# Performance work log

Measured on AMD Instinct MI355X. Metric: run time of the kernel, lower is better.

Reference implementation:

```python
import jax, jax.numpy as jnp
import numpy as np

H = 2  # num_heads hardcoded in the torch module


def setup_inputs() -> dict:
    key = jax.random.key(0)
    ks = jax.random.split(key, 10)
    B, S, D = 8, 2048, 512
    s = 0.02
    return {
        "rgb": jax.random.normal(ks[0], (B, S, D), jnp.float32),
        "event": jax.random.normal(ks[1], (B, S, D), jnp.float32),
        "w_rgb": jax.random.normal(ks[2], (D, D), jnp.float32) * s,
        "b_rgb": jnp.zeros((D,), jnp.float32),
        "w_event": jax.random.normal(ks[3], (D, D), jnp.float32) * s,
        "b_event": jnp.zeros((D,), jnp.float32),
        "w_in": jax.random.normal(ks[4], (3 * D, D), jnp.float32) * s,   # packed QKV in_proj, torch layout
        "b_in": jnp.zeros((3 * D,), jnp.float32),
        "w_out": jax.random.normal(ks[5], (D, D), jnp.float32) * s,
        "b_out": jnp.zeros((D,), jnp.float32),
    }


def _mha(q_in, kv_in, w_in, b_in, w_out, b_out):
    """torch nn.MultiheadAttention with key==value==kv_in, batch-first math."""
    B, S, D = q_in.shape
    hd = D // H
    q = q_in @ w_in[:D].T + b_in[:D]
    k = kv_in @ w_in[D:2 * D].T + b_in[D:2 * D]
    v = kv_in @ w_in[2 * D:].T + b_in[2 * D:]
    q = q.reshape(B, S, H, hd) * (1.0 / np.sqrt(hd))
    k = k.reshape(B, S, H, hd)
    v = v.reshape(B, S, H, hd)
    scores = jnp.einsum('bqhd,bkhd->bhqk', q, k)          # [B,H,S,S]
    attn = jax.nn.softmax(scores, axis=-1)
    out = jnp.einsum('bhqk,bkhd->bqhd', attn, v).reshape(B, S, D)
    return out @ w_out.T + b_out


def reference(rgb, event, w_rgb, b_rgb, w_event, b_event, w_in, b_in, w_out, b_out):
    rgb_p = rgb @ w_rgb.T + b_rgb
    event_p = event @ w_event.T + b_event
    # same attention weights used for both cross directions
    event_attn = _mha(rgb_p, event_p, w_in, b_in, w_out, b_out)
    rgb_attn = _mha(event_p, rgb_p, w_in, b_in, w_out, b_out)
    gate = jax.nn.sigmoid(jnp.sum(rgb_p * event_p, axis=-1, keepdims=True))
    fused = gate * event_attn + (1.0 - gate) * rgb_attn
    return fused + (rgb_p + event_p) * 0.5
```

## Files before the change

kernel.cpp:

```cpp
#include <hip/hip_runtime.h>
#include <hip/hip_bf16.h>
#include <stdint.h>


typedef __bf16 bf16_t;
typedef __bf16 bf16x8 __attribute__((ext_vector_type(8)));
typedef float f32x4 __attribute__((ext_vector_type(4)));
typedef float f32x16 __attribute__((ext_vector_type(16)));
typedef unsigned int u32;
typedef unsigned char u8;

typedef void gvoid_t __attribute__((address_space(1)));
typedef void svoid_t __attribute__((address_space(3)));

__device__ inline void gload16(const void* g, void* l) {
    __builtin_amdgcn_global_load_lds((gvoid_t*)g, (svoid_t*)l, 16, 0, 0);
}

__device__ inline float exp2v(float x) {
    float r;
    asm("v_exp_f32 %0, %1" : "=v"(r) : "v"(x));
    return r;
}

template <bool HI>
__device__ inline u32 pk_fp8(float a, float b, u32 old) {
    return (u32)__builtin_amdgcn_cvt_pk_fp8_f32(a, b, (int)old, HI);
}
__device__ inline u8 to_fp8(float a) { return (u8)(pk_fp8<false>(a, a, 0) & 0xff); }
__device__ inline long pk64(u32 lo, u32 hi) {
    return (long)(((unsigned long long)hi << 32) | (unsigned long long)lo);
}
__device__ inline f32x16 mfma_fp8(long a, long b, f32x16 c) {
    return __builtin_amdgcn_mfma_f32_32x32x16_fp8_fp8(a, b, c, 0, 0, 0);
}

__global__ __launch_bounds__(256) void f2b_w(const float* __restrict__ s2, bf16_t* __restrict__ d2,
                                             const float* __restrict__ s3, bf16_t* __restrict__ d3,
                                             const float* __restrict__ s4, bf16_t* __restrict__ d4,
                                             const float* __restrict__ s5, bf16_t* __restrict__ d5) {
    int i = blockIdx.x * 256 + threadIdx.x;
    const float* s; bf16_t* d; int off;
    if (i < 32768)       { s = s2; d = d2; off = i; }
    else if (i < 65536)  { s = s3; d = d3; off = i - 32768; }
    else if (i < 163840) { s = s4; d = d4; off = i - 65536; }
    else                 { s = s5; d = d5; off = i - 163840; }
    const float4* p = reinterpret_cast<const float4*>(s) + (size_t)off * 2;
    float4 a = p[0], b = p[1];
    bf16x8 o;
    o[0] = (bf16_t)a.x; o[1] = (bf16_t)a.y; o[2] = (bf16_t)a.z; o[3] = (bf16_t)a.w;
    o[4] = (bf16_t)b.x; o[5] = (bf16_t)b.y; o[6] = (bf16_t)b.z; o[7] = (bf16_t)b.w;
    reinterpret_cast<bf16x8*>(d)[off] = o;
}

template <int MODE>
__global__ __launch_bounds__(256) void gemm_bt(const float* __restrict__ Af,
                                               const float* __restrict__ Af2,
                                               const bf16_t* __restrict__ A,
                                               const bf16_t* __restrict__ A2,
                                               const bf16_t* __restrict__ Bw,
                                               const bf16_t* __restrict__ Bw2,
                                               const float* __restrict__ bias,
                                               const float* __restrict__ bias2,
                                               void* __restrict__ Cout,
                                               void* __restrict__ Cout2,
                                               const bf16_t* __restrict__ r1,
                                               const bf16_t* __restrict__ r2,
                                               const float* __restrict__ gate,
                                               u8* __restrict__ qdst,
                                               u8* __restrict__ kdst,
                                               u8* __restrict__ vdst,
                                               u8* __restrict__ qdst2,
                                               u8* __restrict__ kdst2,
                                               u8* __restrict__ vdst2,
                                               int N, int K) {
    __shared__ __align__(16) bf16_t As[128][64];
    __shared__ __align__(16) bf16_t Bs[128][64];
    const int tid = threadIdx.x, lane = tid & 63, w = tid >> 6;
    const int l16 = lane & 15, l4 = lane >> 4;
    const int wm = w >> 1, wn = w & 1;
    int xt, yt;
    if (MODE == 1) {
        int bid = blockIdx.x;
        int xcd = bid & 7, idx = bid >> 3;
        yt = xcd + 8 * (idx / 12);
        xt = idx % 12;
    } else {
        xt = blockIdx.x; yt = blockIdx.y;
    }
    const bool sec = (MODE != 2) && (yt >= 128);
    const size_t a0 = (size_t)(yt & 127) * 128;
    const size_t b0 = (size_t)xt * 128;
    const bf16_t* Ap = sec ? A2 : A;
    const bf16_t* Bp = sec ? Bw2 : Bw;
    const float* Afp = sec ? Af2 : Af;
    const float* bp = sec ? bias2 : bias;
    f32x4 acc[4][4] = {};
    const int srow = w * 32 + (lane >> 3);
    const int scol = (lane & 7) * 8;
    float g4[4];
    if (MODE == 2) {
#pragma unroll
        for (int i = 0; i < 4; ++i) g4[i] = gate[a0 + srow + i * 8];
    }
    for (int kt = 0; kt < K; kt += 64) {
        __syncthreads();
        if (MODE == 0) {
#pragma unroll
            for (int i = 0; i < 4; ++i) {
                const float4* p = reinterpret_cast<const float4*>(
                    Afp + (a0 + srow + i * 8) * (size_t)K + kt + scol);
                float4 x = p[0], y = p[1];
                bf16x8 o;
                o[0] = (bf16_t)x.x; o[1] = (bf16_t)x.y; o[2] = (bf16_t)x.z; o[3] = (bf16_t)x.w;
                o[4] = (bf16_t)y.x; o[5] = (bf16_t)y.y; o[6] = (bf16_t)y.z; o[7] = (bf16_t)y.w;
                *reinterpret_cast<bf16x8*>(&As[srow + i * 8][scol]) = o;
            }
        } else if (MODE == 2) {
#pragma unroll
            for (int i = 0; i < 4; ++i) {
                size_t ro = (a0 + srow + i * 8) * (size_t)K + kt + scol;
                bf16x8 x = *reinterpret_cast<const bf16x8*>(A + ro);
                bf16x8 y = *reinterpret_cast<const bf16x8*>(A2 + ro);
                bf16x8 o;
#pragma unroll
                for (int j = 0; j < 8; ++j)
                    o[j] = (bf16_t)(g4[i] * (float)x[j] + (1.f - g4[i]) * (float)y[j]);
                *reinterpret_cast<bf16x8*>(&As[srow + i * 8][scol]) = o;
            }
        } else {
#pragma unroll
            for (int i = 0; i < 4; ++i)
                gload16(Ap + (a0 + srow + i * 8) * (size_t)K + kt + scol, &As[w * 32 + i * 8][0]);
        }
#pragma unroll
        for (int i = 0; i < 4; ++i)
            gload16(Bp + (b0 + srow + i * 8) * (size_t)K + kt + scol, &Bs[w * 32 + i * 8][0]);
        __syncthreads();
#pragma unroll
        for (int kk = 0; kk < 2; ++kk) {
            bf16x8 af[4], bfr[4];
#pragma unroll
            for (int mi = 0; mi < 4; ++mi)
                af[mi] = *reinterpret_cast<const bf16x8*>(&As[wm * 64 + mi * 16 + l16][kk * 32 + l4 * 8]);
#pragma unroll
            for (int ni = 0; ni < 4; ++ni)
                bfr[ni] = *reinterpret_cast<const bf16x8*>(&Bs[wn * 64 + ni * 16 + l16][kk * 32 + l4 * 8]);
#pragma unroll
            for (int mi = 0; mi < 4; ++mi)
#pragma unroll
                for (int ni = 0; ni < 4; ++ni)
                    acc[mi][ni] = __builtin_amdgcn_mfma_f32_16x16x32_bf16(af[mi], bfr[ni], acc[mi][ni], 0, 0, 0);
        }
    }
    u8* qd = sec ? qdst2 : qdst;
    u8* kd = sec ? kdst2 : kdst;
    u8* vd = sec ? vdst2 : vdst;
#pragma unroll
    for (int mi = 0; mi < 4; ++mi) {
#pragma unroll
        for (int ni = 0; ni < 4; ++ni) {
            int col = (int)b0 + wn * 64 + ni * 16 + l16;
            float bs = bp[col];
            int row0 = (int)a0 + wm * 64 + mi * 16 + l4 * 4;
            float vv[4];
#pragma unroll
            for (int r = 0; r < 4; ++r) vv[r] = acc[mi][ni][r] + bs;
            if (MODE == 0) {
                bf16_t* Cp = (bf16_t*)(sec ? Cout2 : Cout);
#pragma unroll
                for (int r = 0; r < 4; ++r)
                    Cp[(size_t)(row0 + r) * N + col] = (bf16_t)vv[r];
            } else if (MODE == 2) {
#pragma unroll
                for (int r = 0; r < 4; ++r) {
                    size_t idx = (size_t)(row0 + r) * N + col;
                    ((float*)Cout)[idx] = vv[r] + 0.5f * ((float)r1[idx] + (float)r2[idx]);
                }
            } else {
                if (col < 512) {
#pragma unroll
                    for (int r = 0; r < 4; ++r)
                        qd[(size_t)(row0 + r) * 512 + col] = to_fp8(vv[r]);
                } else if (col < 1024) {
                    int cc = col - 512, hh = cc >> 8, d = cc & 255;
                    int dpart = ((d >> 3) & 1) * 128 + (d >> 4) * 8 + (d & 7);
#pragma unroll
                    for (int r = 0; r < 4; ++r) {
                        int row = row0 + r;
                        int bh = (row >> 11) * 2 + hh, seq = row & 2047;
                        int rr = seq & 31;
                        u32 boff = (u32)(rr * 256 + dpart) ^ (u32)((rr & 7) << 4);
                        kd[((size_t)(bh * 64 + (seq >> 5))) * 8192 + boff] = to_fp8(vv[r]);
                    }
                } else {
                    int cc = col - 1024, hh = cc >> 8, d = cc & 255;
                    int bh = (row0 >> 11) * 2 + hh, seq = row0 & 2047;
                    int k = seq & 31;
                    int s = (k >> 4) & 1, hik = (k >> 3) & 1, j0 = k & 7;
                    u32 wrd = pk_fp8<false>(vv[0], vv[1], 0);
                    wrd = pk_fp8<true>(vv[2], vv[3], wrd);
                    u32 boff = (u32)(d * 32 + hik * 16 + s * 8 + j0) ^ (u32)((d & 7) << 4);
                    *reinterpret_cast<u32*>(vd + ((size_t)(bh * 64 + (seq >> 5))) * 8192 + boff) = wrd;
                }
            }
        }
    }
}

__global__ __launch_bounds__(256) void gate_kernel(const bf16_t* __restrict__ rp,
                                                   const bf16_t* __restrict__ ep,
                                                   float* __restrict__ gate) {
    int row = blockIdx.x * 4 + (threadIdx.x >> 6);
    int lane = threadIdx.x & 63;
    bf16x8 a = reinterpret_cast<const bf16x8*>(rp + (size_t)row * 512)[lane];
    bf16x8 b = reinterpret_cast<const bf16x8*>(ep + (size_t)row * 512)[lane];
    float s = 0.f;
#pragma unroll
    for (int j = 0; j < 8; ++j) s += (float)a[j] * (float)b[j];
#pragma unroll
    for (int off = 32; off; off >>= 1) s += __shfl_xor(s, off, 64);
    if (lane == 0) gate[row] = 1.f / (1.f + __expf(-s));
}

__global__ __launch_bounds__(256, 2) void attn_kernel(const u8* __restrict__ qbr,
                                                      const u8* __restrict__ qbe,
                                                      const u8* __restrict__ kbr,
                                                      const u8* __restrict__ kbe,
                                                      const u8* __restrict__ vbr,
                                                      const u8* __restrict__ vbe,
                                                      bf16_t* __restrict__ out0,
                                                      bf16_t* __restrict__ out1) {
    __shared__ __align__(16) u8 smem[32768];
    const int bid = blockIdx.x;
    const int qb = bid >> 5;
    const int combo = bid & 31;
    const int dir = combo >> 4;
    const int bh = combo & 15;
    const int b = bh >> 1, h = bh & 1;
    const u8* Qb = dir ? qbe : qbr;
    const u8* Kc = dir ? kbr : kbe;
    const u8* Vc = dir ? vbr : vbe;
    bf16_t* osrc = dir ? out1 : out0;
    const int tid = threadIdx.x;
    const int w = tid >> 6, l = tid & 63;
    const int l31 = l & 31, hi = l >> 5;
    const int q0w = qb * 128 + w * 32;

    const u8* qp = Qb + ((size_t)(b * 2048 + q0w + l31)) * 512 + h * 256 + hi * 8;
    uint2 qf[16];
#pragma unroll
    for (int dch = 0; dch < 16; ++dch)
        qf[dch] = *reinterpret_cast<const uint2*>(qp + dch * 16);

    f32x16 O[8] = {};
    float mrun = -1e30f, lrun = 0.f;

    const u8* kq = Kc + (size_t)bh * 524288 + w * 2048 + l * 16;
    const u8* vq = Vc + (size_t)bh * 524288 + w * 2048 + l * 16;

#define STAGE(T, P)                                                          \
    do {                                                                     \
        const u8* ks_ = kq + (size_t)(T) * 8192;                             \
        const u8* vs_ = vq + (size_t)(T) * 8192;                             \
        gload16(ks_, &smem[(P) * 16384 + w * 2048]);                         \
        gload16(ks_ + 1024, &smem[(P) * 16384 + w * 2048 + 1024]);           \
        gload16(vs_, &smem[(P) * 16384 + 8192 + w * 2048]);                  \
        gload16(vs_ + 1024, &smem[(P) * 16384 + 8192 + w * 2048 + 1024]);    \
    } while (0)

    STAGE(0, 0);

    const u32 kx = (u32)((l31 & 7) << 4);
    for (int kt2 = 0; kt2 < 64; ++kt2) {
        asm volatile("s_waitcnt vmcnt(0)" ::: "memory");
        __builtin_amdgcn_s_barrier();
        if (kt2 < 63) STAGE(kt2 + 1, (kt2 + 1) & 1);

        const int cb = kt2 & 1;
        const u8* kbp = &smem[cb * 16384] + l31 * 256 + hi * 128;
        const u8* vg = &smem[cb * 16384 + 8192] + (((u32)(l31 * 32 + hi * 16)) ^ kx);

        f32x16 st = {};
        __builtin_amdgcn_s_setprio(1);
#pragma unroll
        for (int m = 0; m < 8; ++m) {
            uint4 kk = *reinterpret_cast<const uint4*>(kbp + (((u32)(m << 4)) ^ kx));
            st = mfma_fp8(pk64(kk.x, kk.y), pk64(qf[2 * m].x, qf[2 * m].y), st);
            st = mfma_fp8(pk64(kk.z, kk.w), pk64(qf[2 * m + 1].x, qf[2 * m + 1].y), st);
        }
        __builtin_amdgcn_s_setprio(0);

#pragma unroll
        for (int r = 0; r < 16; ++r) st[r] *= 0.090168440f;

        float mx = st[0];
#pragma unroll
        for (int r = 1; r < 16; ++r) mx = fmaxf(mx, st[r]);
        mx = fmaxf(mx, __shfl_xor(mx, 32, 64));
        if (__any(mx - mrun > 8.f)) {
            float mnew = fmaxf(mrun, mx);
            float sc = exp2v(mrun - mnew);
            mrun = mnew;
            lrun *= sc;
#pragma unroll
            for (int r = 0; r < 16; ++r) {
                int qr = (r & 3) + 8 * (r >> 2) + 4 * hi;
                float scr = __shfl(sc, qr, 64);
#pragma unroll
                for (int g = 0; g < 8; ++g) O[g][r] *= scr;
            }
        }
        float p_[16];
        float lsum = 0.f;
#pragma unroll
        for (int r = 0; r < 16; ++r) { p_[r] = exp2v(st[r] - mrun); lsum += p_[r]; }
        lsum += __shfl_xor(lsum, 32, 64);
        lrun += lsum;

        u32 X0 = pk_fp8<false>(p_[0], p_[1], 0);   X0 = pk_fp8<true>(p_[2], p_[3], X0);
        u32 X1 = pk_fp8<false>(p_[4], p_[5], 0);   X1 = pk_fp8<true>(p_[6], p_[7], X1);
        u32 X2 = pk_fp8<false>(p_[8], p_[9], 0);   X2 = pk_fp8<true>(p_[10], p_[11], X2);
        u32 X3 = pk_fp8<false>(p_[12], p_[13], 0); X3 = pk_fp8<true>(p_[14], p_[15], X3);
        u32 E0 = (u32)__shfl_xor((int)(hi ? X0 : X1), 32, 64);
        u32 E1 = (u32)__shfl_xor((int)(hi ? X2 : X3), 32, 64);
        long A0 = pk64(hi ? E0 : X0, hi ? X1 : E0);
        long A1 = pk64(hi ? E1 : X2, hi ? X3 : E1);

        __builtin_amdgcn_s_setprio(1);
#pragma unroll
        for (int g = 0; g < 8; ++g) {
            uint4 v4 = *reinterpret_cast<const uint4*>(vg + g * 1024);
            O[g] = mfma_fp8(A0, pk64(v4.x, v4.y), O[g]);
            O[g] = mfma_fp8(A1, pk64(v4.z, v4.w), O[g]);
        }
        __builtin_amdgcn_s_setprio(0);
    }
#undef STAGE

#pragma unroll
    for (int r = 0; r < 16; ++r) {
        int qr = (r & 3) + 8 * (r >> 2) + 4 * hi;
        float linv = 1.0f / __shfl(lrun, qr, 64);
        size_t rowoff = ((size_t)(b * 2048 + q0w + qr)) * 512 + h * 256 + l31;
#pragma unroll
        for (int g = 0; g < 8; ++g)
            osrc[rowoff + g * 32] = (bf16_t)(O[g][r] * linv);
    }
}

extern "C" void kernel_launch(void* const* d_in, const int* in_sizes, int n_in,
                              void* d_out, int out_size, void* d_ws, size_t ws_size,
                              hipStream_t stream) {
    const float* rgb = (const float*)d_in[0];
    const float* event = (const float*)d_in[1];
    const float* w_rgb = (const float*)d_in[2];
    const float* b_rgb = (const float*)d_in[3];
    const float* w_event = (const float*)d_in[4];
    const float* b_event = (const float*)d_in[5];
    const float* w_in = (const float*)d_in[6];
    const float* b_in = (const float*)d_in[7];
    const float* w_out = (const float*)d_in[8];
    const float* b_out = (const float*)d_in[9];
    float* out = (float*)d_out;

    const size_t MB16 = (size_t)16 * 1024 * 1024;
    char* ws = (char*)d_ws;
    bf16_t* wrgb_bf = (bf16_t*)(ws + 0);
    bf16_t* wevt_bf = (bf16_t*)(ws + 524288);
    bf16_t* wout_bf = (bf16_t*)(ws + 1048576);
    bf16_t* win_bf = (bf16_t*)(ws + 1572864);
    float* gate = (float*)(ws + 3145728);
    bf16_t* bufA = (bf16_t*)(ws + 4194304);
    bf16_t* bufB = (bf16_t*)(ws + 4194304 + MB16);
    bf16_t* rgbp = (bf16_t*)(ws + 4194304 + 2 * MB16);
    bf16_t* evtp = (bf16_t*)(ws + 4194304 + 3 * MB16);
    u8* qbr = (u8*)(ws + 4194304 + 4 * MB16);
    u8* qbe = (u8*)(ws + 4194304 + 5 * MB16);
    u8* kbr = (u8*)(ws + 4194304 + 6 * MB16);
    u8* kbe = (u8*)(ws + 4194304 + 7 * MB16);
    u8* vbr = (u8*)(ws + 4194304 + 8 * MB16);
    u8* vbe = (u8*)(ws + 4194304 + 9 * MB16);

    dim3 blk(256);
    f2b_w<<<768, blk, 0, stream>>>(w_rgb, wrgb_bf, w_event, wevt_bf,
                                   w_in, win_bf, w_out, wout_bf);
    gemm_bt<0><<<dim3(4, 256), blk, 0, stream>>>(rgb, event, nullptr, nullptr,
                                                 wrgb_bf, wevt_bf, b_rgb, b_event,
                                                 rgbp, evtp, nullptr, nullptr, nullptr,
                                                 nullptr, nullptr, nullptr, nullptr, nullptr,
                                                 nullptr, 512, 512);
    gate_kernel<<<4096, blk, 0, stream>>>(rgbp, evtp, gate);
    gemm_bt<1><<<3072, blk, 0, stream>>>(nullptr, nullptr, rgbp, evtp, win_bf, win_bf,
                                         b_in, b_in, nullptr, nullptr, nullptr, nullptr,
                                         nullptr, qbr, kbr, vbr, qbe, kbe, vbe, 1536, 512);
    attn_kernel<<<512, blk, 0, stream>>>(qbr, qbe, kbr, kbe, vbr, vbe, bufA, bufB);
    gemm_bt<2><<<dim3(4, 128), blk, 0, stream>>>(nullptr, nullptr, bufA, bufB, wout_bf, nullptr,
                                                 b_out, nullptr, out, nullptr, rgbp, evtp, gate,
                                                 nullptr, nullptr, nullptr, nullptr, nullptr,
                                                 nullptr, 512, 512);
}
```

Before: 300.9 us.

## Split K and V tile prefetch into separate stages with partial waitcnt

The attention loop now issues the K and V prefetches for the next tile separately instead of as one combined stage. Each phase waits only for the loads it needs (`vmcnt(2)`), so the V load of the current tile can still be in flight while QK^T and softmax run. This hides more global-to-LDS latency behind compute. In exchange it adds a second barrier per iteration and peels off the last iteration.

After: 306.2 us. About the same (+1.8%).

```diff
diff --git a/kernel.cpp b/kernel.cpp
--- a/kernel.cpp
+++ b/kernel.cpp
@@ -259,84 +259,112 @@
     const u8* kq = Kc + (size_t)bh * 524288 + w * 2048 + l * 16;
     const u8* vq = Vc + (size_t)bh * 524288 + w * 2048 + l * 16;
 
-#define STAGE(T, P)                                                          \
+#define SK_(T, P)                                                            \
     do {                                                                     \
         const u8* ks_ = kq + (size_t)(T) * 8192;                             \
-        const u8* vs_ = vq + (size_t)(T) * 8192;                             \
         gload16(ks_, &smem[(P) * 16384 + w * 2048]);                         \
         gload16(ks_ + 1024, &smem[(P) * 16384 + w * 2048 + 1024]);           \
+    } while (0)
+#define SV_(T, P)                                                            \
+    do {                                                                     \
+        const u8* vs_ = vq + (size_t)(T) * 8192;                             \
         gload16(vs_, &smem[(P) * 16384 + 8192 + w * 2048]);                  \
         gload16(vs_ + 1024, &smem[(P) * 16384 + 8192 + w * 2048 + 1024]);    \
     } while (0)
 
-    STAGE(0, 0);
+#define QK_PHASE(CB)                                                          \
+    do {                                                                      \
+        const u8* kbp = &smem[(CB) * 16384] + l31 * 256 + hi * 128;           \
+        __builtin_amdgcn_s_setprio(1);                                        \
+        _Pragma("unroll") for (int m = 0; m < 8; ++m) {                       \
+            uint4 kk = *reinterpret_cast<const uint4*>(kbp + (((u32)(m << 4)) ^ kx)); \
+            st = mfma_fp8(pk64(kk.x, kk.y), pk64(qf[2 * m].x, qf[2 * m].y), st); \
+            st = mfma_fp8(pk64(kk.z, kk.w), pk64(qf[2 * m + 1].x, qf[2 * m + 1].y), st); \
+        }                                                                     \
+        __builtin_amdgcn_s_setprio(0);                                        \
+    } while (0)
+
+#define SOFTMAX_PHASE()                                                       \
+    do {                                                                      \
+        _Pragma("unroll") for (int r = 0; r < 16; ++r) st[r] *= 0.090168440f; \
+        float mx = st[0];                                                     \
+        _Pragma("unroll") for (int r = 1; r < 16; ++r) mx = fmaxf(mx, st[r]); \
+        mx = fmaxf(mx, __shfl_xor(mx, 32, 64));                               \
+        if (__any(mx - mrun > 8.f)) {                                         \
+            float mnew = fmaxf(mrun, mx);                                     \
+            float sc = exp2v(mrun - mnew);                                    \
+            mrun = mnew;                                                      \
+            lrun *= sc;                                                       \
+            _Pragma("unroll") for (int r = 0; r < 16; ++r) {                  \
+                int qr = (r & 3) + 8 * (r >> 2) + 4 * hi;                     \
+                float scr = __shfl(sc, qr, 64);                               \
+                _Pragma("unroll") for (int g = 0; g < 8; ++g) O[g][r] *= scr; \
+            }                                                                 \
+        }                                                                     \
+        float lsum = 0.f;                                                     \
+        _Pragma("unroll") for (int r = 0; r < 16; ++r) {                      \
+            st[r] = exp2v(st[r] - mrun);                                      \
+            lsum += st[r];                                                    \
+        }                                                                     \
+        lsum += __shfl_xor(lsum, 32, 64);                                     \
+        lrun += lsum;                                                         \
+        u32 X0 = pk_fp8<false>(st[0], st[1], 0);   X0 = pk_fp8<true>(st[2], st[3], X0);   \
+        u32 X1 = pk_fp8<false>(st[4], st[5], 0);   X1 = pk_fp8<true>(st[6], st[7], X1);   \
+        u32 X2 = pk_fp8<false>(st[8], st[9], 0);   X2 = pk_fp8<true>(st[10], st[11], X2); \
+        u32 X3 = pk_fp8<false>(st[12], st[13], 0); X3 = pk_fp8<true>(st[14], st[15], X3); \
+        u32 E0 = (u32)__shfl_xor((int)(hi ? X0 : X1), 32, 64);                \
+        u32 E1 = (u32)__shfl_xor((int)(hi ? X2 : X3), 32, 64);                \
+        A0 = pk64(hi ? E0 : X0, hi ? X1 : E0);                                \
+        A1 = pk64(hi ? E1 : X2, hi ? X3 : E1);                                \
+    } while (0)
+
+#define PV_PHASE(CB)                                                          \
+    do {                                                                      \
+        const u8* vg = &smem[(CB) * 16384 + 8192] + (((u32)(l31 * 32 + hi * 16)) ^ kx); \
+        __builtin_amdgcn_s_setprio(1);                                        \
+        _Pragma("unroll") for (int g = 0; g < 8; ++g) {                       \
+            uint4 v4 = *reinterpret_cast<const uint4*>(vg + g * 1024);        \
+            O[g] = mfma_fp8(A0, pk64(v4.x, v4.y), O[g]);                      \
+            O[g] = mfma_fp8(A1, pk64(v4.z, v4.w), O[g]);                      \
+        }                                                                     \
+        __builtin_amdgcn_s_setprio(0);                                        \
+    } while (0)
 
     const u32 kx = (u32)((l31 & 7) << 4);
-    for (int kt2 = 0; kt2 < 64; ++kt2) {
+    long A0, A1;
+
+    SK_(0, 0);
+    SV_(0, 0);
+
+    for (int kt2 = 0; kt2 < 63; ++kt2) {
+        const int cb = kt2 & 1, nb = (kt2 + 1) & 1;
+        asm volatile("s_waitcnt vmcnt(2)" ::: "memory");
+        __builtin_amdgcn_s_barrier();
+        SK_(kt2 + 1, nb);
+        f32x16 st = {};
+        QK_PHASE(cb);
+        SOFTMAX_PHASE();
+        asm volatile("s_waitcnt vmcnt(2)" ::: "memory");
+        __builtin_amdgcn_s_barrier();
+        SV_(kt2 + 1, nb);
+        PV_PHASE(cb);
+    }
+    {
+        const int cb = 63 & 1;
+        asm volatile("s_waitcnt vmcnt(2)" ::: "memory");
+        __builtin_amdgcn_s_barrier();
+        f32x16 st = {};
+        QK_PHASE(cb);
+        SOFTMAX_PHASE();
         asm volatile("s_waitcnt vmcnt(0)" ::: "memory");
         __builtin_amdgcn_s_barrier();
-        if (kt2 < 63) STAGE(kt2 + 1, (kt2 + 1) & 1);
-
-        const int cb = kt2 & 1;
-        const u8* kbp = &smem[cb * 16384] + l31 * 256 + hi * 128;
-        const u8* vg = &smem[cb * 16384 + 8192] + (((u32)(l31 * 32 + hi * 16)) ^ kx);
-
-        f32x16 st = {};
-        __builtin_amdgcn_s_setprio(1);
-#pragma unroll
-        for (int m = 0; m < 8; ++m) {
-            uint4 kk = *reinterpret_cast<const uint4*>(kbp + (((u32)(m << 4)) ^ kx));
-            st = mfma_fp8(pk64(kk.x, kk.y), pk64(qf[2 * m].x, qf[2 * m].y), st);
-            st = mfma_fp8(pk64(kk.z, kk.w), pk64(qf[2 * m + 1].x, qf[2 * m + 1].y), st);
-        }
-        __builtin_amdgcn_s_setprio(0);
-
-#pragma unroll
-        for (int r = 0; r < 16; ++r) st[r] *= 0.090168440f;
-
-        float mx = st[0];
-#pragma unroll
-        for (int r = 1; r < 16; ++r) mx = fmaxf(mx, st[r]);
-        mx = fmaxf(mx, __shfl_xor(mx, 32, 64));
-        if (__any(mx - mrun > 8.f)) {
-            float mnew = fmaxf(mrun, mx);
-            float sc = exp2v(mrun - mnew);
-            mrun = mnew;
-            lrun *= sc;
-#pragma unroll
-            for (int r = 0; r < 16; ++r) {
-                int qr = (r & 3) + 8 * (r >> 2) + 4 * hi;
-                float scr = __shfl(sc, qr, 64);
-#pragma unroll
-                for (int g = 0; g < 8; ++g) O[g][r] *= scr;
-            }
-        }
-        float p_[16];
-        float lsum = 0.f;
-#pragma unroll
-        for (int r = 0; r < 16; ++r) { p_[r] = exp2v(st[r] - mrun); lsum += p_[r]; }
-        lsum += __shfl_xor(lsum, 32, 64);
-        lrun += lsum;
-
-        u32 X0 = pk_fp8<false>(p_[0], p_[1], 0);   X0 = pk_fp8<true>(p_[2], p_[3], X0);
-        u32 X1 = pk_fp8<false>(p_[4], p_[5], 0);   X1 = pk_fp8<true>(p_[6], p_[7], X1);
-        u32 X2 = pk_fp8<false>(p_[8], p_[9], 0);   X2 = pk_fp8<true>(p_[10], p_[11], X2);
-        u32 X3 = pk_fp8<false>(p_[12], p_[13], 0); X3 = pk_fp8<true>(p_[14], p_[15], X3);
-        u32 E0 = (u32)__shfl_xor((int)(hi ? X0 : X1), 32, 64);
-        u32 E1 = (u32)__shfl_xor((int)(hi ? X2 : X3), 32, 64);
-        long A0 = pk64(hi ? E0 : X0, hi ? X1 : E0);
-        long A1 = pk64(hi ? E1 : X2, hi ? X3 : E1);
-
-        __builtin_amdgcn_s_setprio(1);
-#pragma unroll
-        for (int g = 0; g < 8; ++g) {
-            uint4 v4 = *reinterpret_cast<const uint4*>(vg + g * 1024);
-            O[g] = mfma_fp8(A0, pk64(v4.x, v4.y), O[g]);
-            O[g] = mfma_fp8(A1, pk64(v4.z, v4.w), O[g]);
-        }
-        __builtin_amdgcn_s_setprio(0);
-    }
-#undef STAGE
+        PV_PHASE(cb);
+    }
+#undef SK_
+#undef SV_
+#undef QK_PHASE
+#undef SOFTMAX_PHASE
+#undef PV_PHASE
 
 #pragma unroll
     for (int r = 0; r < 16; ++r) {
```
